# Optimization experiments

Hardware: AMD Instinct MI355X
Metric: run time of the kernel (lower is better)

Reference implementation:

```python
import jax, jax.numpy as jnp
import numpy as np

B, IN_CH, OUT_CH, ZDIM, KSZ, WH = 16, 64, 64, 64, 3, 32
T, K = 32768, 128


def setup_inputs() -> dict:
    key = jax.random.key(0)
    ks = jax.random.split(key, 10)
    bound = float(np.sqrt(6.0 / OUT_CH))
    return {
        "x": jax.random.normal(ks[0], (B, IN_CH, T), jnp.float32),
        "z": jax.random.normal(ks[1], (B, ZDIM, K), jnp.float32),
        # weight_model: conv1x1(ZDIM->WH), ReLU, conv1x1(WH->IN_CH*OUT_CH*KSZ)
        "wm1": jax.random.normal(ks[2], (WH, ZDIM), jnp.float32) * 0.1,
        "wb1": jnp.zeros((WH,), jnp.float32),
        "wm2": jax.random.normal(ks[3], (IN_CH * OUT_CH * KSZ, WH), jnp.float32) * 0.02,
        "wb2": jnp.zeros((IN_CH * OUT_CH * KSZ,), jnp.float32),
        # bias_model: conv1x1(ZDIM->WH), ReLU, conv1x1(WH->OUT_CH)
        "bm1": jax.random.normal(ks[4], (WH, ZDIM), jnp.float32) * 0.1,
        "bb1": jnp.zeros((WH,), jnp.float32),
        "bm2": jax.random.normal(ks[5], (OUT_CH, WH), jnp.float32) * 0.1,
        "bb2": jnp.zeros((OUT_CH,), jnp.float32),
        # residual / skip 1x1 convs (uniform init per module)
        "rw": jax.random.uniform(ks[6], (OUT_CH, OUT_CH), jnp.float32, -bound, bound),
        "rb": jnp.zeros((OUT_CH,), jnp.float32),
        "sw": jax.random.uniform(ks[7], (OUT_CH, OUT_CH), jnp.float32, -bound, bound),
        "sb": jnp.zeros((OUT_CH,), jnp.float32),
    }


def reference(x, z, wm1, wb1, wm2, wb2, bm1, bb1, bm2, bb2, rw, rb, sw, sb):
    Bq, Cin, Tq = x.shape
    Kq = z.shape[-1]
    S = Tq // Kq  # samples per segment

    # hypernet: per-segment weights, shape (B, Cin*KSZ*OUT_CH, K)
    h = jax.nn.relu(jnp.einsum('hz,bzk->bhk', wm1, z) + wb1[None, :, None])
    w = jnp.einsum('oh,bhk->bok', wm2, h) + wb2[None, :, None]
    # (B, Cin*KSZ, OUT_CH, K) -> (B, K, KSZ, Cin, OUT_CH)
    w = w.reshape(Bq, KSZ, Cin, OUT_CH, Kq).transpose(0, 4, 1, 2, 3)
    # torch cat concatenates KSZ identical copies of x along channels (the
    # dilation shifts are absent in the source), so summing the weight over
    w_eff = w.sum(axis=2)  # (B, K, Cin, OUT_CH)

    hb = jax.nn.relu(jnp.einsum('hz,bzk->bhk', bm1, z) + bb1[None, :, None])
    b = jnp.einsum('oh,bhk->bok', bm2, hb) + bb2[None, :, None]  # (B, OUT_CH, K)
    b = b.transpose(0, 2, 1)  # (B, K, OUT_CH)

    # per-segment batched matmul
    xr = x.transpose(0, 2, 1).reshape(Bq, Kq, S, Cin)
    y = jnp.einsum('bksi,bkio->bkso', xr, w_eff) + b[:, :, None, :]
    y = jnp.sin(y.reshape(Bq, Tq, OUT_CH).transpose(0, 2, 1))  # (B, OUT_CH, T)

    residual = jnp.einsum('oc,bct->bot', rw, y) + rb[None, :, None]
    skip = jnp.einsum('oc,bct->bot', sw, y) + sb[None, :, None]
    return (residual + x) / 2, skip
```

## Files before the change

### kernel.cpp

```cpp
#include <hip/hip_runtime.h>
#include <hip/hip_bf16.h>

#define B_    16
#define CIN   64
#define COUT  64
#define ZD    64
#define WHID  32
#define TT    32768
#define KK    128
#define SS    256

__global__ void k_tapsum(const float* __restrict__ wm2, float* __restrict__ wm2s) {
    int i = blockIdx.x * 256 + threadIdx.x;
    if (i < 4096 * 32)
        wm2s[i] = wm2[i] + wm2[i + 131072] + wm2[i + 262144];
}

__global__ __launch_bounds__(256) void k_hyper_small(
    const float* __restrict__ z,
    const float* __restrict__ wm1, const float* __restrict__ wb1,
    const float* __restrict__ bm1, const float* __restrict__ bb1,
    const float* __restrict__ bm2, const float* __restrict__ bb2,
    float* __restrict__ ws_h, float* __restrict__ ws_bias)
{
    __shared__ float hb[8][32];
    const int tid = threadIdx.x;
    const int seg = tid >> 5, w = tid & 31;
    const int bk = blockIdx.x * 8 + seg;
    const int b = bk >> 7, k = bk & 127;
    const float* zp = z + b * ZD * KK + k;

    float hv = wb1[w], hbv = bb1[w];
    #pragma unroll
    for (int zz = 0; zz < 64; ++zz) {
        float zv = zp[zz * KK];
        hv  += wm1[w * 64 + zz] * zv;
        hbv += bm1[w * 64 + zz] * zv;
    }
    hv  = fmaxf(hv, 0.f);
    hbv = fmaxf(hbv, 0.f);
    ws_h[bk * 32 + w] = hv;
    hb[seg][w] = hbv;
    __syncthreads();

    #pragma unroll
    for (int t = 0; t < 2; ++t) {
        int o = w + t * 32;
        float acc = bb2[o];
        #pragma unroll
        for (int hh = 0; hh < 32; ++hh)
            acc += bm2[o * 32 + hh] * hb[seg][hh];
        ws_bias[bk * 64 + o] = acc;
    }
}

__global__ __launch_bounds__(256) void k_weff(
    const float* __restrict__ wm2s, const float* __restrict__ wb2,
    const float* __restrict__ ws_h, float* __restrict__ ws_w)
{
    const int tid = threadIdx.x;
    const int wave = tid >> 6, lane = tid & 63;
    const int bk = blockIdx.x * 4 + wave;

    float hreg[32];
    #pragma unroll
    for (int hh = 0; hh < 32; ++hh)
        hreg[hh] = ws_h[bk * 32 + hh];

    for (int jj = 0; jj < 64; ++jj) {
        int j = jj * 64 + lane;
        float4 row[8];
        const float4* rp = (const float4*)(wm2s + j * 32);
        #pragma unroll
        for (int q = 0; q < 8; ++q) row[q] = rp[q];
        float wb = wb2[j] + wb2[j + 4096] + wb2[j + 8192];
        const float* rowf = (const float*)row;
        float acc = wb;
        #pragma unroll
        for (int hh = 0; hh < 32; ++hh)
            acc += rowf[hh] * hreg[hh];
        ws_w[(size_t)bk * 4096 + j] = acc;
    }
}

__global__ __launch_bounds__(512, 4) void k_main(
    const float* __restrict__ x,
    const float* __restrict__ ws_w, const float* __restrict__ ws_bias,
    const float* __restrict__ rw, const float* __restrict__ rb,
    const float* __restrict__ sw, const float* __restrict__ sb,
    float* __restrict__ out)
{
    __shared__ float U[8192];
    __shared__ __align__(16) unsigned short ybuf[64][256];

    const int tid = threadIdx.x;
    const int bk = blockIdx.x;
    const int b = bk >> 7, k = bk & 127;
    const int tbase = k * SS;
    const int sg = tid & 63, og = tid >> 6;
    const int s0 = sg * 4, o0 = og * 8;
    float4* U4 = (float4*)U;

    {
        const float4* Wg = (const float4*)(ws_w + (size_t)bk * 4096);
        #pragma unroll
        for (int r = 0; r < 2; ++r) U4[tid + 512 * r] = Wg[tid + 512 * r];
        if (tid < 64) U[4096 + tid] = ws_bias[bk * 64 + tid];
    }
    __syncthreads();

    float acc[4][8];
    #pragma unroll
    for (int e = 0; e < 4; ++e)
        #pragma unroll
        for (int v = 0; v < 8; ++v) acc[e][v] = 0.f;

    const float* xs = x + (size_t)b * CIN * TT + tbase + s0;
    #pragma unroll 8
    for (int i = 0; i < 64; ++i) {
        float4 xv = *(const float4*)(xs + (size_t)i * TT);
        #pragma unroll
        for (int q = 0; q < 2; ++q) {
            float4 wq = U4[i * 16 + og * 2 + q];
            float wv[4] = {wq.x, wq.y, wq.z, wq.w};
            #pragma unroll
            for (int e2 = 0; e2 < 4; ++e2) {
                acc[0][q * 4 + e2] += xv.x * wv[e2];
                acc[1][q * 4 + e2] += xv.y * wv[e2];
                acc[2][q * 4 + e2] += xv.z * wv[e2];
                acc[3][q * 4 + e2] += xv.w * wv[e2];
            }
        }
    }

    float rgv[8], sgv[8];
    #pragma unroll
    for (int r = 0; r < 8; ++r) {
        int idx = r * 512 + tid;
        int o = idx & 63, c = idx >> 6;
        rgv[r] = rw[o * 64 + c];
        sgv[r] = sw[o * 64 + c];
    }

    #pragma unroll
    for (int v = 0; v < 8; ++v) {
        int o = o0 + v;
        float bo = U[4096 + o];
        unsigned int us[4];
        #pragma unroll
        for (int e = 0; e < 4; ++e) {
            float yv = __sinf(acc[e][v] + bo);
            unsigned int u = __float_as_uint(yv);
            u += 0x7fffu + ((u >> 16) & 1u);
            us[e] = u >> 16;
        }
        uint2 pk;
        pk.x = us[0] | (us[1] << 16);
        pk.y = us[2] | (us[3] << 16);
        *(uint2*)&ybuf[o][s0] = pk;
    }
    __syncthreads();

    #pragma unroll
    for (int r = 0; r < 8; ++r) {
        int idx = r * 512 + tid;
        int o = idx & 63, c = idx >> 6;
        U[c * 64 + o]        = rgv[r];
        U[4096 + c * 64 + o] = sgv[r];
    }
    __syncthreads();

    float ar[4][8], asx[4][8];
    #pragma unroll
    for (int e = 0; e < 4; ++e)
        #pragma unroll
        for (int v = 0; v < 8; ++v) { ar[e][v] = 0.f; asx[e][v] = 0.f; }

    #pragma unroll 4
    for (int c = 0; c < 64; ++c) {
        uint2 yu = *(const uint2*)&ybuf[c][s0];
        float yv[4];
        yv[0] = __uint_as_float(yu.x << 16);
        yv[1] = __uint_as_float(yu.x & 0xffff0000u);
        yv[2] = __uint_as_float(yu.y << 16);
        yv[3] = __uint_as_float(yu.y & 0xffff0000u);
        #pragma unroll
        for (int q = 0; q < 2; ++q) {
            float4 rq = U4[c * 16 + og * 2 + q];
            float4 sq = U4[1024 + c * 16 + og * 2 + q];
            float rv[4] = {rq.x, rq.y, rq.z, rq.w};
            float sv[4] = {sq.x, sq.y, sq.z, sq.w};
            #pragma unroll
            for (int e2 = 0; e2 < 4; ++e2) {
                #pragma unroll
                for (int e = 0; e < 4; ++e) {
                    ar[e][q * 4 + e2]  += yv[e] * rv[e2];
                    asx[e][q * 4 + e2] += yv[e] * sv[e2];
                }
            }
        }
    }

    float* resp = out;
    float* skpp = out + (size_t)B_ * COUT * TT;
    #pragma unroll
    for (int v = 0; v < 8; ++v) {
        int o = o0 + v;
        size_t off = (size_t)(b * COUT + o) * TT + tbase + s0;
        float4 xo = *(const float4*)(x + off);
        float rbv = rb[o], sbv = sb[o];
        float4 ro, so;
        ro.x = (ar[0][v] + rbv + xo.x) * 0.5f;
        ro.y = (ar[1][v] + rbv + xo.y) * 0.5f;
        ro.z = (ar[2][v] + rbv + xo.z) * 0.5f;
        ro.w = (ar[3][v] + rbv + xo.w) * 0.5f;
        so.x = asx[0][v] + sbv;
        so.y = asx[1][v] + sbv;
        so.z = asx[2][v] + sbv;
        so.w = asx[3][v] + sbv;
        *(float4*)(resp + off) = ro;
        *(float4*)(skpp + off) = so;
    }
}

extern "C" void kernel_launch(void* const* d_in, const int* in_sizes, int n_in,
                              void* d_out, int out_size, void* d_ws, size_t ws_size,
                              hipStream_t stream) {
    const float* x   = (const float*)d_in[0];
    const float* z   = (const float*)d_in[1];
    const float* wm1 = (const float*)d_in[2];
    const float* wb1 = (const float*)d_in[3];
    const float* wm2 = (const float*)d_in[4];
    const float* wb2 = (const float*)d_in[5];
    const float* bm1 = (const float*)d_in[6];
    const float* bb1 = (const float*)d_in[7];
    const float* bm2 = (const float*)d_in[8];
    const float* bb2 = (const float*)d_in[9];
    const float* rw  = (const float*)d_in[10];
    const float* rb  = (const float*)d_in[11];
    const float* sw  = (const float*)d_in[12];
    const float* sb  = (const float*)d_in[13];
    float* out = (float*)d_out;

    float* ws      = (float*)d_ws;
    float* ws_wm2s = ws;
    float* ws_h    = ws + 131072;
    float* ws_bias = ws + 196608;
    float* ws_w    = ws + 327680;

    hipLaunchKernelGGL(k_tapsum, dim3(512), dim3(256), 0, stream, wm2, ws_wm2s);
    hipLaunchKernelGGL(k_hyper_small, dim3(256), dim3(256), 0, stream,
                       z, wm1, wb1, bm1, bb1, bm2, bb2, ws_h, ws_bias);
    hipLaunchKernelGGL(k_weff, dim3(512), dim3(256), 0, stream,
                       ws_wm2s, wb2, ws_h, ws_w);
    hipLaunchKernelGGL(k_main, dim3(2048), dim3(512), 0, stream,
                       x, ws_w, ws_bias, rw, rb, sw, sb, out);
}
```

Measured before the change: 648.3 us.

## Fuse per-segment weight generation into main kernel and double-buffer x loads

Result: faster. 572.5 us (-11.7%).

```diff
diff --git a/kernel.cpp b/kernel.cpp
--- a/kernel.cpp
+++ b/kernel.cpp
@@ -10,10 +10,13 @@
 #define KK    128
 #define SS    256
 
-__global__ void k_tapsum(const float* __restrict__ wm2, float* __restrict__ wm2s) {
+__global__ void k_tapsum(const float* __restrict__ wm2, const float* __restrict__ wb2,
+                         float* __restrict__ wm2s, float* __restrict__ wbs) {
     int i = blockIdx.x * 256 + threadIdx.x;
     if (i < 4096 * 32)
         wm2s[i] = wm2[i] + wm2[i + 131072] + wm2[i + 262144];
+    if (i < 4096)
+        wbs[i] = wb2[i] + wb2[i + 4096] + wb2[i + 8192];
 }
 
 __global__ __launch_bounds__(256) void k_hyper_small(
@@ -54,38 +57,10 @@
     }
 }
 
-__global__ __launch_bounds__(256) void k_weff(
-    const float* __restrict__ wm2s, const float* __restrict__ wb2,
-    const float* __restrict__ ws_h, float* __restrict__ ws_w)
-{
-    const int tid = threadIdx.x;
-    const int wave = tid >> 6, lane = tid & 63;
-    const int bk = blockIdx.x * 4 + wave;
-
-    float hreg[32];
-    #pragma unroll
-    for (int hh = 0; hh < 32; ++hh)
-        hreg[hh] = ws_h[bk * 32 + hh];
-
-    for (int jj = 0; jj < 64; ++jj) {
-        int j = jj * 64 + lane;
-        float4 row[8];
-        const float4* rp = (const float4*)(wm2s + j * 32);
-        #pragma unroll
-        for (int q = 0; q < 8; ++q) row[q] = rp[q];
-        float wb = wb2[j] + wb2[j + 4096] + wb2[j + 8192];
-        const float* rowf = (const float*)row;
-        float acc = wb;
-        #pragma unroll
-        for (int hh = 0; hh < 32; ++hh)
-            acc += rowf[hh] * hreg[hh];
-        ws_w[(size_t)bk * 4096 + j] = acc;
-    }
-}
-
 __global__ __launch_bounds__(512, 4) void k_main(
     const float* __restrict__ x,
-    const float* __restrict__ ws_w, const float* __restrict__ ws_bias,
+    const float* __restrict__ wm2s, const float* __restrict__ wbs,
+    const float* __restrict__ ws_h, const float* __restrict__ ws_bias,
     const float* __restrict__ rw, const float* __restrict__ rb,
     const float* __restrict__ sw, const float* __restrict__ sb,
     float* __restrict__ out)
@@ -101,11 +76,32 @@
     const int s0 = sg * 4, o0 = og * 8;
     float4* U4 = (float4*)U;
 
+    const float* xs = x + (size_t)b * CIN * TT + tbase + s0;
+    float4 xbA[4], xbB[4];
+    #pragma unroll
+    for (int r = 0; r < 4; ++r)
+        xbA[r] = *(const float4*)(xs + (size_t)r * TT);
+
     {
-        const float4* Wg = (const float4*)(ws_w + (size_t)bk * 4096);
-        #pragma unroll
-        for (int r = 0; r < 2; ++r) U4[tid + 512 * r] = Wg[tid + 512 * r];
+        float hreg[32];
+        #pragma unroll
+        for (int hh = 0; hh < 32; ++hh) hreg[hh] = ws_h[bk * 32 + hh];
         if (tid < 64) U[4096 + tid] = ws_bias[bk * 64 + tid];
+
+        #pragma unroll
+        for (int r = 0; r < 8; ++r) {
+            const int j = r * 512 + tid;
+            const float4* rp = (const float4*)(wm2s + j * 32);
+            float4 row[8];
+            #pragma unroll
+            for (int q = 0; q < 8; ++q) row[q] = rp[q];
+            const float* rowf = (const float*)row;
+            float a = wbs[j];
+            #pragma unroll
+            for (int hh = 0; hh < 32; ++hh)
+                a += rowf[hh] * hreg[hh];
+            U[j] = a;
+        }
     }
     __syncthreads();
 
@@ -115,20 +111,30 @@
         #pragma unroll
         for (int v = 0; v < 8; ++v) acc[e][v] = 0.f;
 
-    const float* xs = x + (size_t)b * CIN * TT + tbase + s0;
-    #pragma unroll 8
-    for (int i = 0; i < 64; ++i) {
-        float4 xv = *(const float4*)(xs + (size_t)i * TT);
-        #pragma unroll
-        for (int q = 0; q < 2; ++q) {
-            float4 wq = U4[i * 16 + og * 2 + q];
-            float wv[4] = {wq.x, wq.y, wq.z, wq.w};
-            #pragma unroll
-            for (int e2 = 0; e2 < 4; ++e2) {
-                acc[0][q * 4 + e2] += xv.x * wv[e2];
-                acc[1][q * 4 + e2] += xv.y * wv[e2];
-                acc[2][q * 4 + e2] += xv.z * wv[e2];
-                acc[3][q * 4 + e2] += xv.w * wv[e2];
+    #pragma unroll
+    for (int jb = 0; jb < 16; ++jb) {
+        if (jb < 15) {
+            #pragma unroll
+            for (int r = 0; r < 4; ++r) {
+                float4 v = *(const float4*)(xs + (size_t)((jb + 1) * 4 + r) * TT);
+                if ((jb & 1) == 0) xbB[r] = v; else xbA[r] = v;
+            }
+        }
+        #pragma unroll
+        for (int r = 0; r < 4; ++r) {
+            float4 xv = ((jb & 1) == 0) ? xbA[r] : xbB[r];
+            const int c = jb * 4 + r;
+            #pragma unroll
+            for (int q = 0; q < 2; ++q) {
+                float4 wq = U4[c * 16 + og * 2 + q];
+                float wv[4] = {wq.x, wq.y, wq.z, wq.w};
+                #pragma unroll
+                for (int e2 = 0; e2 < 4; ++e2) {
+                    acc[0][q * 4 + e2] += xv.x * wv[e2];
+                    acc[1][q * 4 + e2] += xv.y * wv[e2];
+                    acc[2][q * 4 + e2] += xv.z * wv[e2];
+                    acc[3][q * 4 + e2] += xv.w * wv[e2];
+                }
             }
         }
     }
@@ -244,15 +250,13 @@
 
     float* ws      = (float*)d_ws;
     float* ws_wm2s = ws;
-    float* ws_h    = ws + 131072;
-    float* ws_bias = ws + 196608;
-    float* ws_w    = ws + 327680;
-
-    hipLaunchKernelGGL(k_tapsum, dim3(512), dim3(256), 0, stream, wm2, ws_wm2s);
+    float* ws_wbs  = ws + 131072;
+    float* ws_h    = ws + 135168;
+    float* ws_bias = ws + 200704;
+
+    hipLaunchKernelGGL(k_tapsum, dim3(512), dim3(256), 0, stream, wm2, wb2, ws_wm2s, ws_wbs);
     hipLaunchKernelGGL(k_hyper_small, dim3(256), dim3(256), 0, stream,
                        z, wm1, wb1, bm1, bb1, bm2, bb2, ws_h, ws_bias);
-    hipLaunchKernelGGL(k_weff, dim3(512), dim3(256), 0, stream,
-                       ws_wm2s, wb2, ws_h, ws_w);
     hipLaunchKernelGGL(k_main, dim3(2048), dim3(512), 0, stream,
-                       x, ws_w, ws_bias, rw, rb, sw, sb, out);
-}
+                       x, ws_wm2s, ws_wbs, ws_h, ws_bias, rw, rb, sw, sb, out);
+}
```

## Restructure weight hypernet kernel for row reuse and use packed fp32 FMAs

Applied to the files above, without the earlier changes.

Result: faster. 524.0 us (-19.2%).

```diff
diff --git a/kernel.cpp b/kernel.cpp
--- a/kernel.cpp
+++ b/kernel.cpp
@@ -10,10 +10,15 @@
 #define KK    128
 #define SS    256
 
-__global__ void k_tapsum(const float* __restrict__ wm2, float* __restrict__ wm2s) {
+typedef float f2 __attribute__((ext_vector_type(2)));
+
+__global__ void k_tapsum(const float* __restrict__ wm2, const float* __restrict__ wb2,
+                         float* __restrict__ wm2s, float* __restrict__ wbs) {
     int i = blockIdx.x * 256 + threadIdx.x;
     if (i < 4096 * 32)
         wm2s[i] = wm2[i] + wm2[i + 131072] + wm2[i + 262144];
+    if (i < 4096)
+        wbs[i] = wb2[i] + wb2[i + 4096] + wb2[i + 8192];
 }
 
 __global__ __launch_bounds__(256) void k_hyper_small(
@@ -54,32 +59,35 @@
     }
 }
 
-__global__ __launch_bounds__(256) void k_weff(
-    const float* __restrict__ wm2s, const float* __restrict__ wb2,
+__global__ __launch_bounds__(256, 2) void k_weff(
+    const float* __restrict__ wm2s, const float* __restrict__ wbs,
     const float* __restrict__ ws_h, float* __restrict__ ws_w)
 {
+    __shared__ float hsh[64 * 32];
     const int tid = threadIdx.x;
-    const int wave = tid >> 6, lane = tid & 63;
-    const int bk = blockIdx.x * 4 + wave;
-
-    float hreg[32];
-    #pragma unroll
-    for (int hh = 0; hh < 32; ++hh)
-        hreg[hh] = ws_h[bk * 32 + hh];
-
-    for (int jj = 0; jj < 64; ++jj) {
-        int j = jj * 64 + lane;
-        float4 row[8];
-        const float4* rp = (const float4*)(wm2s + j * 32);
-        #pragma unroll
-        for (int q = 0; q < 8; ++q) row[q] = rp[q];
-        float wb = wb2[j] + wb2[j + 4096] + wb2[j + 8192];
-        const float* rowf = (const float*)row;
+    const int jt = blockIdx.x & 15, bt = blockIdx.x >> 4;
+    const int j = jt * 256 + tid;
+    const int bk0 = bt * 64;
+
+    #pragma unroll
+    for (int r = 0; r < 8; ++r)
+        hsh[r * 256 + tid] = ws_h[bk0 * 32 + r * 256 + tid];
+
+    float4 row[8];
+    const float4* rp = (const float4*)(wm2s + j * 32);
+    #pragma unroll
+    for (int q = 0; q < 8; ++q) row[q] = rp[q];
+    const float* rowf = (const float*)row;
+    const float wb = wbs[j];
+    __syncthreads();
+
+    #pragma unroll 4
+    for (int bk = 0; bk < 64; ++bk) {
         float acc = wb;
         #pragma unroll
         for (int hh = 0; hh < 32; ++hh)
-            acc += rowf[hh] * hreg[hh];
-        ws_w[(size_t)bk * 4096 + j] = acc;
+            acc += rowf[hh] * hsh[bk * 32 + hh];
+        ws_w[(size_t)(bk0 + bk) * 4096 + j] = acc;
     }
 }
 
@@ -109,27 +117,30 @@
     }
     __syncthreads();
 
-    float acc[4][8];
+    f2 acc2[4][4];
     #pragma unroll
     for (int e = 0; e < 4; ++e)
         #pragma unroll
-        for (int v = 0; v < 8; ++v) acc[e][v] = 0.f;
+        for (int p = 0; p < 4; ++p) { f2 zz = {0.f, 0.f}; acc2[e][p] = zz; }
 
     const float* xs = x + (size_t)b * CIN * TT + tbase + s0;
     #pragma unroll 8
     for (int i = 0; i < 64; ++i) {
         float4 xv = *(const float4*)(xs + (size_t)i * TT);
+        f2 xs0 = {xv.x, xv.x}, xs1 = {xv.y, xv.y};
+        f2 xs2 = {xv.z, xv.z}, xs3 = {xv.w, xv.w};
         #pragma unroll
         for (int q = 0; q < 2; ++q) {
             float4 wq = U4[i * 16 + og * 2 + q];
-            float wv[4] = {wq.x, wq.y, wq.z, wq.w};
-            #pragma unroll
-            for (int e2 = 0; e2 < 4; ++e2) {
-                acc[0][q * 4 + e2] += xv.x * wv[e2];
-                acc[1][q * 4 + e2] += xv.y * wv[e2];
-                acc[2][q * 4 + e2] += xv.z * wv[e2];
-                acc[3][q * 4 + e2] += xv.w * wv[e2];
-            }
+            f2 w0 = {wq.x, wq.y}, w1 = {wq.z, wq.w};
+            acc2[0][q * 2]     += xs0 * w0;
+            acc2[0][q * 2 + 1] += xs0 * w1;
+            acc2[1][q * 2]     += xs1 * w0;
+            acc2[1][q * 2 + 1] += xs1 * w1;
+            acc2[2][q * 2]     += xs2 * w0;
+            acc2[2][q * 2 + 1] += xs2 * w1;
+            acc2[3][q * 2]     += xs3 * w0;
+            acc2[3][q * 2 + 1] += xs3 * w1;
         }
     }
 
@@ -149,7 +160,7 @@
         unsigned int us[4];
         #pragma unroll
         for (int e = 0; e < 4; ++e) {
-            float yv = __sinf(acc[e][v] + bo);
+            float yv = __sinf(acc2[e][v >> 1][v & 1] + bo);
             unsigned int u = __float_as_uint(yv);
             u += 0x7fffu + ((u >> 16) & 1u);
             us[e] = u >> 16;
@@ -170,34 +181,42 @@
     }
     __syncthreads();
 
-    float ar[4][8], asx[4][8];
+    f2 ar2[4][4], as2[4][4];
     #pragma unroll
     for (int e = 0; e < 4; ++e)
         #pragma unroll
-        for (int v = 0; v < 8; ++v) { ar[e][v] = 0.f; asx[e][v] = 0.f; }
+        for (int p = 0; p < 4; ++p) { f2 zz = {0.f, 0.f}; ar2[e][p] = zz; as2[e][p] = zz; }
 
     #pragma unroll 4
     for (int c = 0; c < 64; ++c) {
         uint2 yu = *(const uint2*)&ybuf[c][s0];
-        float yv[4];
-        yv[0] = __uint_as_float(yu.x << 16);
-        yv[1] = __uint_as_float(yu.x & 0xffff0000u);
-        yv[2] = __uint_as_float(yu.y << 16);
-        yv[3] = __uint_as_float(yu.y & 0xffff0000u);
+        float y0 = __uint_as_float(yu.x << 16);
+        float y1 = __uint_as_float(yu.x & 0xffff0000u);
+        float y2 = __uint_as_float(yu.y << 16);
+        float y3 = __uint_as_float(yu.y & 0xffff0000u);
+        f2 d0 = {y0, y0}, d1 = {y1, y1}, d2 = {y2, y2}, d3 = {y3, y3};
         #pragma unroll
         for (int q = 0; q < 2; ++q) {
             float4 rq = U4[c * 16 + og * 2 + q];
             float4 sq = U4[1024 + c * 16 + og * 2 + q];
-            float rv[4] = {rq.x, rq.y, rq.z, rq.w};
-            float sv[4] = {sq.x, sq.y, sq.z, sq.w};
-            #pragma unroll
-            for (int e2 = 0; e2 < 4; ++e2) {
-                #pragma unroll
-                for (int e = 0; e < 4; ++e) {
-                    ar[e][q * 4 + e2]  += yv[e] * rv[e2];
-                    asx[e][q * 4 + e2] += yv[e] * sv[e2];
-                }
-            }
+            f2 r0 = {rq.x, rq.y}, r1 = {rq.z, rq.w};
+            f2 v0 = {sq.x, sq.y}, v1 = {sq.z, sq.w};
+            ar2[0][q * 2]     += d0 * r0;
+            ar2[0][q * 2 + 1] += d0 * r1;
+            ar2[1][q * 2]     += d1 * r0;
+            ar2[1][q * 2 + 1] += d1 * r1;
+            ar2[2][q * 2]     += d2 * r0;
+            ar2[2][q * 2 + 1] += d2 * r1;
+            ar2[3][q * 2]     += d3 * r0;
+            ar2[3][q * 2 + 1] += d3 * r1;
+            as2[0][q * 2]     += d0 * v0;
+            as2[0][q * 2 + 1] += d0 * v1;
+            as2[1][q * 2]     += d1 * v0;
+            as2[1][q * 2 + 1] += d1 * v1;
+            as2[2][q * 2]     += d2 * v0;
+            as2[2][q * 2 + 1] += d2 * v1;
+            as2[3][q * 2]     += d3 * v0;
+            as2[3][q * 2 + 1] += d3 * v1;
         }
     }
 
@@ -210,14 +229,14 @@
         float4 xo = *(const float4*)(x + off);
         float rbv = rb[o], sbv = sb[o];
         float4 ro, so;
-        ro.x = (ar[0][v] + rbv + xo.x) * 0.5f;
-        ro.y = (ar[1][v] + rbv + xo.y) * 0.5f;
-        ro.z = (ar[2][v] + rbv + xo.z) * 0.5f;
-        ro.w = (ar[3][v] + rbv + xo.w) * 0.5f;
-        so.x = asx[0][v] + sbv;
-        so.y = asx[1][v] + sbv;
-        so.z = asx[2][v] + sbv;
-        so.w = asx[3][v] + sbv;
+        ro.x = (ar2[0][v >> 1][v & 1] + rbv + xo.x) * 0.5f;
+        ro.y = (ar2[1][v >> 1][v & 1] + rbv + xo.y) * 0.5f;
+        ro.z = (ar2[2][v >> 1][v & 1] + rbv + xo.z) * 0.5f;
+        ro.w = (ar2[3][v >> 1][v & 1] + rbv + xo.w) * 0.5f;
+        so.x = as2[0][v >> 1][v & 1] + sbv;
+        so.y = as2[1][v >> 1][v & 1] + sbv;
+        so.z = as2[2][v >> 1][v & 1] + sbv;
+        so.w = as2[3][v >> 1][v & 1] + sbv;
         *(float4*)(resp + off) = ro;
         *(float4*)(skpp + off) = so;
     }
@@ -244,15 +263,16 @@
 
     float* ws      = (float*)d_ws;
     float* ws_wm2s = ws;
-    float* ws_h    = ws + 131072;
-    float* ws_bias = ws + 196608;
-    float* ws_w    = ws + 327680;
-
-    hipLaunchKernelGGL(k_tapsum, dim3(512), dim3(256), 0, stream, wm2, ws_wm2s);
+    float* ws_wbs  = ws + 131072;
+    float* ws_h    = ws + 135168;
+    float* ws_bias = ws + 200704;
+    float* ws_w    = ws + 331776;
+
+    hipLaunchKernelGGL(k_tapsum, dim3(512), dim3(256), 0, stream, wm2, wb2, ws_wm2s, ws_wbs);
     hipLaunchKernelGGL(k_hyper_small, dim3(256), dim3(256), 0, stream,
                        z, wm1, wb1, bm1, bb1, bm2, bb2, ws_h, ws_bias);
     hipLaunchKernelGGL(k_weff, dim3(512), dim3(256), 0, stream,
-                       ws_wm2s, wb2, ws_h, ws_w);
+                       ws_wm2s, ws_wbs, ws_h, ws_w);
     hipLaunchKernelGGL(k_main, dim3(2048), dim3(512), 0, stream,
                        x, ws_w, ws_bias, rw, rb, sw, sb, out);
 }
```
